# Performance work log

Hardware: AMD Instinct MI355X
Metric: run time of the kernel (lower is better)

Reference implementation:

```python
import jax, jax.numpy as jnp
import numpy as np

B, S, D, H, M = 4, 512, 768, 12, 4
DFF = 4 * D
HD = D // H
EPS = 1e-6  # timm/jvp_layers LayerNorm eps
SCALE = HD ** -0.5


def _ln(x, g, b):
    mu = jnp.mean(x, axis=-1, keepdims=True)
    var = jnp.mean((x - mu) ** 2, axis=-1, keepdims=True)
    return (x - mu) * jax.lax.rsqrt(var + EPS) * g + b


def _block(x, g1, b1, Wqkv, Wproj, bproj, g2, b2, W1, bf1, W2, bf2):
    # pre-norm attention
    h = _ln(x, g1, b1)
    qkv = h @ Wqkv                       # [B,S,3D]
    q, k, v = jnp.split(qkv, 3, axis=-1)
    q = q.reshape(B, S, H, HD)
    k = k.reshape(B, S, H, HD)
    v = v.reshape(B, S, H, HD)
    scores = jnp.einsum('bqhd,bkhd->bhqk', q, k) * SCALE
    attn = jax.nn.softmax(scores, axis=-1)
    o = jnp.einsum('bhqk,bkhd->bqhd', attn, v).reshape(B, S, D)
    x = x + o @ Wproj + bproj
    # pre-norm MLP
    h2 = _ln(x, g2, b2)
    mlp = jax.nn.gelu(h2 @ W1 + bf1, approximate=False) @ W2 + bf2
    return x + mlp


def setup_inputs() -> dict:
    key = jax.random.key(0)
    ks = jax.random.split(key, 8)
    w = 0.02
    return {
        'x': jax.random.normal(ks[0], (B, S, D), jnp.float32),
        'x_tangent': jax.random.normal(ks[1], (B, M, S, D), jnp.float32),
        'g1': jnp.ones((D,), jnp.float32),
        'b1': jnp.zeros((D,), jnp.float32),
        'Wqkv': jax.random.normal(ks[2], (D, 3 * D), jnp.float32) * w,
        'Wproj': jax.random.normal(ks[3], (D, D), jnp.float32) * w,
        'bproj': jnp.zeros((D,), jnp.float32),
        'g2': jnp.ones((D,), jnp.float32),
        'b2': jnp.zeros((D,), jnp.float32),
        'W1': jax.random.normal(ks[4], (D, DFF), jnp.float32) * w,
        'bf1': jnp.zeros((DFF,), jnp.float32),
        'W2': jax.random.normal(ks[5], (DFF, D), jnp.float32) * w,
        'bf2': jnp.zeros((D,), jnp.float32),
    }


def reference(x, x_tangent, g1, b1, Wqkv, Wproj, bproj, g2, b2, W1, bf1, W2, bf2):
    f = lambda xx: _block(xx, g1, b1, Wqkv, Wproj, bproj, g2, b2, W1, bf1, W2, bf2)
    # linearize once: primal + efficient JVP for all M tangent directions
    out, jvp_fn = jax.linearize(f, x)
    out_tangent = jax.vmap(jvp_fn, in_axes=1, out_axes=1)(x_tangent)  # [B,M,S,D]
    return out, out_tangent
```

## Files before the change

### kernel.cpp

```cpp
#include <hip/hip_runtime.h>
#include <math.h>

constexpr int B_ = 4, S_ = 512, D_ = 768, H_ = 12, M_ = 4, DFF_ = 3072, HD_ = 64;
constexpr float EPS_ = 1e-6f;
constexpr float SCALE_ = 0.125f;
constexpr int BS_ = B_ * S_;
constexpr int BH_ = B_ * H_;
constexpr long long BSD_ = (long long)BS_ * D_;
constexpr long long BS3D_ = (long long)BS_ * 3 * D_;
constexpr long long ATT_ = (long long)BH_ * S_ * S_;
constexpr long long BSF_ = (long long)BS_ * DFF_;

typedef __attribute__((ext_vector_type(8))) short bf16x8;
typedef __attribute__((ext_vector_type(4))) float f32x4;

__device__ __forceinline__ ushort f2bf(float f) {
    uint32_t u = __float_as_uint(f);
    u += 0x7FFF + ((u >> 16) & 1);
    return (ushort)(u >> 16);
}
__device__ __forceinline__ float bf2f(ushort u) {
    return __uint_as_float((uint32_t)u << 16);
}

__device__ __forceinline__ void gll16(const ushort* g, ushort* l) {
    __builtin_amdgcn_global_load_lds((const __attribute__((address_space(1))) void*)g,
                                     (__attribute__((address_space(3))) void*)l, 16, 0, 0);
}

template <int N> __device__ __forceinline__ void waitcnt_vm() {
    if constexpr (N == 0) asm volatile("s_waitcnt vmcnt(0)" ::: "memory");
    else if constexpr (N == 4) asm volatile("s_waitcnt vmcnt(4)" ::: "memory");
    else if constexpr (N == 6) asm volatile("s_waitcnt vmcnt(6)" ::: "memory");
    else if constexpr (N == 8) asm volatile("s_waitcnt vmcnt(8)" ::: "memory");
    else static_assert(N == 0 || N == 4 || N == 6 || N == 8, "add literal");
}

__device__ __forceinline__ void waitcnt_lgkm0() {
    asm volatile("s_waitcnt lgkmcnt(0)" ::: "memory");
    __builtin_amdgcn_sched_barrier(0);
}

__device__ __forceinline__ int xcd_swz(int flat, int nwg) {
    int q = nwg >> 3, r = nwg & 7;
    int x = flat & 7, pos = flat >> 3;
    int base = (x < r) ? x * (q + 1) : r * (q + 1) + (x - r) * q;
    return base + pos;
}

__device__ __forceinline__ size_t stroff(int rg, int c, int Nc) {
    int m = rg >> 11;
    int b = (rg >> 9) & (B_ - 1);
    int s = rg & (S_ - 1);
    return ((size_t)((b * M_ + m) * S_ + s)) * Nc + c;
}

__device__ __forceinline__ float block_sum(float v) {
    __shared__ float red[4];
    int tid = threadIdx.x;
#pragma unroll
    for (int off = 32; off > 0; off >>= 1) v += __shfl_down(v, off, 64);
    __syncthreads();
    if ((tid & 63) == 0) red[tid >> 6] = v;
    __syncthreads();
    return red[0] + red[1] + red[2] + red[3];
}

__device__ __forceinline__ float block_max(float v) {
    __shared__ float red[4];
    int tid = threadIdx.x;
#pragma unroll
    for (int off = 32; off > 0; off >>= 1) v = fmaxf(v, __shfl_down(v, off, 64));
    __syncthreads();
    if ((tid & 63) == 0) red[tid >> 6] = v;
    __syncthreads();
    return fmaxf(fmaxf(red[0], red[1]), fmaxf(red[2], red[3]));
}

__global__ __launch_bounds__(256) void transpose_f2b(const float* __restrict__ W,
                                                     ushort* __restrict__ WT,
                                                     int K, int N) {
    __shared__ float t[32][33];
    int n0 = blockIdx.x * 32, k0 = blockIdx.y * 32;
    int tx = threadIdx.x & 31, ty = threadIdx.x >> 5;
#pragma unroll
    for (int i = 0; i < 4; i++)
        t[ty + i * 8][tx] = W[(size_t)(k0 + ty + i * 8) * N + n0 + tx];
    __syncthreads();
#pragma unroll
    for (int i = 0; i < 4; i++)
        WT[(size_t)(n0 + ty + i * 8) * K + k0 + tx] = f2bf(t[tx][ty + i * 8]);
}

__global__ __launch_bounds__(256) void transpose_v(const ushort* __restrict__ src0,
                                                   ushort* __restrict__ dst0) {
    int z = blockIdx.z;
    int m = z / BH_, bh = z % BH_;
    const ushort* qkvb = src0 + (size_t)m * BS3D_;
    ushort* Vt = dst0 + (size_t)m * BSD_;
    int b = bh / H_, hh = bh - b * H_;
    int s0 = blockIdx.x * 32, d0 = blockIdx.y * 32;
    __shared__ ushort t[32][33];
    int tx = threadIdx.x & 31, ty = threadIdx.x >> 5;
#pragma unroll
    for (int i = 0; i < 4; i++)
        t[ty + i * 8][tx] = qkvb[(size_t)(b * S_ + s0 + ty + i * 8) * 3 * D_ + 2 * D_ + hh * HD_ + d0 + tx];
    __syncthreads();
#pragma unroll
    for (int i = 0; i < 4; i++)
        Vt[(size_t)bh * HD_ * S_ + (size_t)(d0 + ty + i * 8) * S_ + s0 + tx] = t[tx][ty + i * 8];
}

__global__ __launch_bounds__(256) void ln_fwd(const float* __restrict__ x,
                                              const float* __restrict__ g,
                                              const float* __restrict__ bta,
                                              ushort* __restrict__ xhat,
                                              ushort* __restrict__ h,
                                              float* __restrict__ rstd) {
    int row = blockIdx.x;
    const float* xr = x + (size_t)row * D_;
    int tid = threadIdx.x;
    float v[3];
    float s = 0.f;
#pragma unroll
    for (int i = 0; i < 3; i++) { v[i] = xr[tid + i * 256]; s += v[i]; }
    s = block_sum(s);
    float mu = s * (1.0f / D_);
    float vs = 0.f;
#pragma unroll
    for (int i = 0; i < 3; i++) { float c = v[i] - mu; vs += c * c; }
    vs = block_sum(vs);
    float rs = rsqrtf(vs * (1.0f / D_) + EPS_);
#pragma unroll
    for (int i = 0; i < 3; i++) {
        int c = tid + i * 256;
        float xh = (v[i] - mu) * rs;
        xhat[(size_t)row * D_ + c] = f2bf(xh);
        h[(size_t)row * D_ + c] = f2bf(xh * g[c] + bta[c]);
    }
    if (tid == 0) rstd[row] = rs;
}

__global__ __launch_bounds__(256) void ln_jvp(const float* __restrict__ tf,
                                              const ushort* __restrict__ tb, int mode,
                                              const ushort* __restrict__ xhat,
                                              const float* __restrict__ rstd,
                                              const float* __restrict__ g,
                                              ushort* __restrict__ dh) {
    int rg = blockIdx.x;
    int r = rg & (BS_ - 1);
    size_t pbase = (size_t)r * D_;
    int tid = threadIdx.x;
    float tv[3], xh[3];
    float s1 = 0.f, s2 = 0.f;
    size_t tbase;
    if (mode == 0) {
        int m = rg >> 11;
        int b = r >> 9, s = r & (S_ - 1);
        tbase = ((size_t)((b * M_ + m) * S_ + s)) * D_;
    } else {
        tbase = (size_t)rg * D_;
    }
#pragma unroll
    for (int i = 0; i < 3; i++) {
        int c = tid + i * 256;
        tv[i] = (mode == 0) ? tf[tbase + c] : bf2f(tb[tbase + c]);
        xh[i] = bf2f(xhat[pbase + c]);
        s1 += tv[i];
        s2 += tv[i] * xh[i];
    }
    s1 = block_sum(s1);
    s2 = block_sum(s2);
    float mt = s1 * (1.0f / D_);
    float mx = s2 * (1.0f / D_);
    float rs = rstd[r];
#pragma unroll
    for (int i = 0; i < 3; i++) {
        int c = tid + i * 256;
        dh[(size_t)rg * D_ + c] = f2bf(g[c] * rs * (tv[i] - mt - xh[i] * mx));
    }
}

template <int BM, int BN, int EPI, bool RS, bool OS>
__global__ __launch_bounds__(256) void gemm_mfma(const ushort* __restrict__ A,
                                                 const ushort* __restrict__ BT,
                                                 const float* __restrict__ bias,
                                                 const float* __restrict__ resf,
                                                 const ushort* __restrict__ resb,
                                                 float* __restrict__ Cf,
                                                 ushort* __restrict__ Cb,
                                                 ushort* __restrict__ aux,
                                                 int Nc, int Kd) {
    constexpr int FI = BM / 32, FJ = BN / 32;
    constexpr int LA = BM / 32, LB = BN / 32, L = LA + LB;
    __shared__ ushort As[2][BM * 64];
    __shared__ ushort Bs[2][BN * 64];
    int tid = threadIdx.x;
    int wave = tid >> 6, lane = tid & 63;
    int wr = wave >> 1, wc = wave & 1;
    int gx = gridDim.x, nwg = gx * gridDim.y;
    int work = xcd_swz(blockIdx.x + blockIdx.y * gx, nwg);
    int band = work / (8 * gx);
    int wi = work - band * (8 * gx);
    int row0 = (band * 8 + (wi & 7)) * BM;
    int col0 = (wi >> 3) * BN;

    int srow = lane >> 3;
    int skel = ((lane & 7) ^ (lane >> 3)) * 8;
    const ushort* Ag0 = A + (size_t)(row0 + srow) * Kd + skel;
    const ushort* Bg0 = BT + (size_t)(col0 + srow) * Kd + skel;

    auto stage = [&](int bufi, int k0) {
#pragma unroll
        for (int cc = 0; cc < LA; cc++) {
            int c = wave * LA + cc;
            gll16(Ag0 + (size_t)(c * 8) * Kd + k0, As[bufi] + c * 512);
        }
#pragma unroll
        for (int cc = 0; cc < LB; cc++) {
            int c = wave * LB + cc;
            gll16(Bg0 + (size_t)(c * 8) * Kd + k0, Bs[bufi] + c * 512);
        }
    };

    int frow = lane & 15, fkb = (lane >> 4) * 8;
    int aoff[2][FI], boff[2][FJ];
#pragma unroll
    for (int ks = 0; ks < 2; ks++) {
        int sw = (fkb + ks * 32) ^ ((frow & 7) * 8);
#pragma unroll
        for (int i = 0; i < FI; i++) aoff[ks][i] = (wr * (BM / 2) + i * 16 + frow) * 64 + sw;
#pragma unroll
        for (int j = 0; j < FJ; j++) boff[ks][j] = (wc * (BN / 2) + j * 16 + frow) * 64 + sw;
    }

    f32x4 acc[FI][FJ] = {};

    int nt = Kd >> 6;
    stage(0, 0);
    if (nt > 1) { stage(1, 64); waitcnt_vm<L>(); }
    else        { waitcnt_vm<0>(); }
    __builtin_amdgcn_s_barrier();
    __builtin_amdgcn_sched_barrier(0);

    int cur = 0;
    for (int t = 0; t < nt; t++) {
        bf16x8 af[2][FI], bfv[2][FJ];
        const ushort* Ab = As[cur];
        const ushort* Bb = Bs[cur];
#pragma unroll
        for (int ks = 0; ks < 2; ks++) {
#pragma unroll
            for (int i = 0; i < FI; i++) af[ks][i] = *(const bf16x8*)(Ab + aoff[ks][i]);
#pragma unroll
            for (int j = 0; j < FJ; j++) bfv[ks][j] = *(const bf16x8*)(Bb + boff[ks][j]);
        }
        waitcnt_lgkm0();
        __builtin_amdgcn_s_barrier();
        if (t + 2 < nt) {
            stage(cur, (t + 2) << 6);
            __builtin_amdgcn_sched_barrier(0);
        }
#pragma unroll
        for (int ks = 0; ks < 2; ks++)
#pragma unroll
            for (int i = 0; i < FI; i++)
#pragma unroll
                for (int j = 0; j < FJ; j++)
                    acc[i][j] = __builtin_amdgcn_mfma_f32_16x16x32_bf16(af[ks][i], bfv[ks][j], acc[i][j], 0, 0, 0);
        __builtin_amdgcn_sched_barrier(0);
        if (t + 2 < nt) waitcnt_vm<L>();
        else if (t + 1 < nt) waitcnt_vm<0>();
        __builtin_amdgcn_s_barrier();
        __builtin_amdgcn_sched_barrier(0);
        cur ^= 1;
    }

#pragma unroll
    for (int i = 0; i < FI; i++) {
        int rbase = row0 + wr * (BM / 2) + i * 16 + (lane >> 4) * 4;
#pragma unroll
        for (int j = 0; j < FJ; j++) {
            int c = col0 + wc * (BN / 2) + j * 16 + (lane & 15);
#pragma unroll
            for (int r = 0; r < 4; r++) {
                int rg = rbase + r;
                size_t off = (size_t)rg * Nc + c;
                float v = acc[i][j][r];
                if (EPI == 0) {
                    if (bias) v += bias[c];
                    if (resf) v += resf[RS ? stroff(rg, c, Nc) : off];
                    if (resb) v += bf2f(resb[off]);
                    if (Cf) { if (OS) Cf[stroff(rg, c, Nc)] = v; else Cf[off] = v; }
                    if (Cb) Cb[off] = f2bf(v);
                } else if (EPI == 1) {
                    v += bias[c];
                    float cdf = 0.5f * (1.0f + erff(v * 0.70710678118654752f));
                    Cb[off] = f2bf(v * cdf);
                    aux[off] = f2bf(cdf + v * 0.39894228040143267f * expf(-0.5f * v * v));
                } else {
                    Cb[off] = f2bf(v * bf2f(aux[(size_t)(rg & (BS_ - 1)) * Nc + c]));
                }
            }
        }
    }
}

template <bool TAN>
__global__ __launch_bounds__(256) void attn_qk_mfma(const ushort* __restrict__ qkvb,
                                                    const ushort* __restrict__ dqkvp,
                                                    ushort* __restrict__ sc) {
    int work = xcd_swz(blockIdx.x, gridDim.x);
    constexpr int NT = S_ / 128;
    int mz = work / (BH_ * NT * NT);
    int rem = work % (BH_ * NT * NT);
    int bh = rem / (NT * NT);
    int r2 = rem % (NT * NT);
    int q0 = (r2 / NT) * 128, kc0 = (r2 % NT) * 128;
    int b = bh / H_, hh = bh - b * H_;
    const size_t qoff = (size_t)b * S_ * 3 * D_ + hh * HD_;
    const int ld = 3 * D_;
    const ushort* dqkv = TAN ? dqkvp + (size_t)mz * BS3D_ : nullptr;
    __shared__ ushort As[128 * 64];
    __shared__ ushort Bs[128 * 64];
    __shared__ ushort dAs[TAN ? 128 * 64 : 1];
    __shared__ ushort dBs[TAN ? 128 * 64 : 1];
    int tid = threadIdx.x;
    int wave = tid >> 6, lane = tid & 63;
    int wr = wave >> 1, wc = wave & 1;

    int srow = lane >> 3;
    int skel = ((lane & 7) ^ (lane >> 3)) * 8;
    const ushort* Ag0 = qkvb + qoff + (size_t)(q0 + srow) * ld + skel;
    const ushort* Bg0 = qkvb + qoff + D_ + (size_t)(kc0 + srow) * ld + skel;

#pragma unroll
    for (int cc = 0; cc < 4; cc++) {
        int c = wave * 4 + cc;
        gll16(Ag0 + (size_t)(c * 8) * ld, As + c * 512);
        gll16(Bg0 + (size_t)(c * 8) * ld, Bs + c * 512);
        if (TAN) {
            gll16(dqkv + qoff + (size_t)(q0 + c * 8 + srow) * ld + skel, dAs + c * 512);
            gll16(dqkv + qoff + D_ + (size_t)(kc0 + c * 8 + srow) * ld + skel, dBs + c * 512);
        }
    }
    __syncthreads();

    int frow = lane & 15, fkb = (lane >> 4) * 8;
    f32x4 acc[4][4] = {};
#pragma unroll
    for (int ks = 0; ks < 2; ks++) {
        int sw = (fkb + ks * 32) ^ ((frow & 7) * 8);
        bf16x8 af[4], bfv[4];
#pragma unroll
        for (int i = 0; i < 4; i++) af[i] = *(const bf16x8*)(As + (wr * 64 + i * 16 + frow) * 64 + sw);
#pragma unroll
        for (int j = 0; j < 4; j++) bfv[j] = *(const bf16x8*)(Bs + (wc * 64 + j * 16 + frow) * 64 + sw);
        if (!TAN) {
#pragma unroll
            for (int i = 0; i < 4; i++)
#pragma unroll
                for (int j = 0; j < 4; j++)
                    acc[i][j] = __builtin_amdgcn_mfma_f32_16x16x32_bf16(af[i], bfv[j], acc[i][j], 0, 0, 0);
        } else {
            bf16x8 daf[4], dbf[4];
#pragma unroll
            for (int i = 0; i < 4; i++) daf[i] = *(const bf16x8*)(dAs + (wr * 64 + i * 16 + frow) * 64 + sw);
#pragma unroll
            for (int j = 0; j < 4; j++) dbf[j] = *(const bf16x8*)(dBs + (wc * 64 + j * 16 + frow) * 64 + sw);
#pragma unroll
            for (int i = 0; i < 4; i++)
#pragma unroll
                for (int j = 0; j < 4; j++) {
                    acc[i][j] = __builtin_amdgcn_mfma_f32_16x16x32_bf16(daf[i], bfv[j], acc[i][j], 0, 0, 0);
                    acc[i][j] = __builtin_amdgcn_mfma_f32_16x16x32_bf16(af[i], dbf[j], acc[i][j], 0, 0, 0);
                }
        }
    }

    ushort* scm = sc + (size_t)mz * ATT_;
#pragma unroll
    for (int i = 0; i < 4; i++) {
        int rbase = q0 + wr * 64 + i * 16 + (lane >> 4) * 4;
#pragma unroll
        for (int j = 0; j < 4; j++) {
            int c = kc0 + wc * 64 + j * 16 + (lane & 15);
#pragma unroll
            for (int r = 0; r < 4; r++)
                scm[((size_t)bh * S_ + rbase + r) * S_ + c] = f2bf(acc[i][j][r] * SCALE_);
        }
    }
}

__global__ __launch_bounds__(256) void attn_av_p(const ushort* __restrict__ Pb,
                                                 const ushort* __restrict__ Vt,
                                                 ushort* __restrict__ outp) {
    int work = xcd_swz(blockIdx.x, gridDim.x);
    constexpr int NT = S_ / 128;
    int bh = work / NT;
    int q0 = (work % NT) * 128;
    int b = bh / H_, hh = bh - b * H_;
    const ushort* Pg = Pb + (size_t)bh * S_ * S_;
    const ushort* Vg = Vt + (size_t)bh * HD_ * S_;
    __shared__ ushort As[128 * 64];
    __shared__ ushort Bs[64 * 64];
    int tid = threadIdx.x;
    int wave = tid >> 6, lane = tid & 63;
    int wr = wave >> 1, wc = wave & 1;
    int srow = lane >> 3;
    int skel = ((lane & 7) ^ (lane >> 3)) * 8;
    int frow = lane & 15, fkb = (lane >> 4) * 8;

    f32x4 acc[4][2] = {};
    for (int k0 = 0; k0 < S_; k0 += 64) {
#pragma unroll
        for (int cc = 0; cc < 4; cc++) {
            int c = wave * 4 + cc;
            gll16(Pg + (size_t)(q0 + c * 8 + srow) * S_ + k0 + skel, As + c * 512);
        }
#pragma unroll
        for (int cc = 0; cc < 2; cc++) {
            int c = wave * 2 + cc;
            gll16(Vg + (size_t)(c * 8 + srow) * S_ + k0 + skel, Bs + c * 512);
        }
        __syncthreads();
#pragma unroll
        for (int ks = 0; ks < 2; ks++) {
            int sw = (fkb + ks * 32) ^ ((frow & 7) * 8);
            bf16x8 af[4], bfv[2];
#pragma unroll
            for (int i = 0; i < 4; i++) af[i] = *(const bf16x8*)(As + (wr * 64 + i * 16 + frow) * 64 + sw);
#pragma unroll
            for (int j = 0; j < 2; j++) bfv[j] = *(const bf16x8*)(Bs + (wc * 32 + j * 16 + frow) * 64 + sw);
#pragma unroll
            for (int i = 0; i < 4; i++)
#pragma unroll
                for (int j = 0; j < 2; j++)
                    acc[i][j] = __builtin_amdgcn_mfma_f32_16x16x32_bf16(af[i], bfv[j], acc[i][j], 0, 0, 0);
        }
        __syncthreads();
    }

#pragma unroll
    for (int i = 0; i < 4; i++) {
        int rbase = q0 + wr * 64 + i * 16 + (lane >> 4) * 4;
#pragma unroll
        for (int j = 0; j < 2; j++) {
            int c = hh * HD_ + wc * 32 + j * 16 + (lane & 15);
#pragma unroll
            for (int r = 0; r < 4; r++)
                outp[(size_t)(b * S_ + rbase + r) * D_ + c] = f2bf(acc[i][j][r]);
        }
    }
}

__global__ __launch_bounds__(256) void attn_av_tan(const ushort* __restrict__ Pb,
                                                   const ushort* __restrict__ dscp,
                                                   const ushort* __restrict__ Vt,
                                                   const ushort* __restrict__ dVtp,
                                                   const ushort* __restrict__ Ob,
                                                   ushort* __restrict__ outp) {
    int work = xcd_swz(blockIdx.x, gridDim.x);
    int mz = work / (BH_ * 4);
    int rem = work % (BH_ * 4);
    int bh = rem / 4;
    int q0 = (rem % 4) * 128;
    int b = bh / H_, hh = bh - b * H_;
    const ushort* Pg = Pb + (size_t)bh * S_ * S_;
    const ushort* Dg = dscp + (size_t)mz * ATT_ + (size_t)bh * S_ * S_;
    const ushort* Vg = Vt + (size_t)bh * HD_ * S_;
    const ushort* dVg = dVtp + (size_t)mz * BSD_ + (size_t)bh * HD_ * S_;
    ushort* outm = outp + (size_t)mz * BSD_;
    __shared__ ushort Ps[128 * 64], Ds[128 * 64], Vs[64 * 64], dVs[64 * 64];
    int tid = threadIdx.x;
    int wave = tid >> 6, lane = tid & 63;
    int wr = wave >> 1, wc = wave & 1;
    int srow = lane >> 3;
    int skel = ((lane & 7) ^ (lane >> 3)) * 8;
    int frow = lane & 15, fkb = (lane >> 4) * 8;
    int aoff[2][4], boff[2][2];
#pragma unroll
    for (int ks = 0; ks < 2; ks++) {
        int sw = (fkb + ks * 32) ^ ((frow & 7) * 8);
#pragma unroll
        for (int i = 0; i < 4; i++) aoff[ks][i] = (wr * 64 + i * 16 + frow) * 64 + sw;
#pragma unroll
        for (int j = 0; j < 2; j++) boff[ks][j] = (wc * 32 + j * 16 + frow) * 64 + sw;
    }

    float s[4] = {0.f, 0.f, 0.f, 0.f};
    f32x4 acc[4][2] = {};

    for (int k0 = 0; k0 < S_; k0 += 64) {
#pragma unroll
        for (int cc = 0; cc < 4; cc++) {
            int c = wave * 4 + cc;
            gll16(Pg + (size_t)(q0 + c * 8 + srow) * S_ + k0 + skel, Ps + c * 512);
            gll16(Dg + (size_t)(q0 + c * 8 + srow) * S_ + k0 + skel, Ds + c * 512);
        }
#pragma unroll
        for (int cc = 0; cc < 2; cc++) {
            int c = wave * 2 + cc;
            gll16(Vg + (size_t)(c * 8 + srow) * S_ + k0 + skel, Vs + c * 512);
            gll16(dVg + (size_t)(c * 8 + srow) * S_ + k0 + skel, dVs + c * 512);
        }
        __syncthreads();
#pragma unroll
        for (int ks = 0; ks < 2; ks++) {
            bf16x8 p8[4], pq8[4], v8[2], dv8[2];
#pragma unroll
            for (int i = 0; i < 4; i++) {
                p8[i] = *(const bf16x8*)(Ps + aoff[ks][i]);
                bf16x8 d8 = *(const bf16x8*)(Ds + aoff[ks][i]);
#pragma unroll
                for (int e = 0; e < 8; e++) {
                    float pd = bf2f((ushort)p8[i][e]) * bf2f((ushort)d8[e]);
                    s[i] += pd;
                    pq8[i][e] = (short)f2bf(pd);
                }
            }
#pragma unroll
            for (int j = 0; j < 2; j++) {
                v8[j] = *(const bf16x8*)(Vs + boff[ks][j]);
                dv8[j] = *(const bf16x8*)(dVs + boff[ks][j]);
            }
#pragma unroll
            for (int i = 0; i < 4; i++)
#pragma unroll
                for (int j = 0; j < 2; j++) {
                    acc[i][j] = __builtin_amdgcn_mfma_f32_16x16x32_bf16(pq8[i], v8[j], acc[i][j], 0, 0, 0);
                    acc[i][j] = __builtin_amdgcn_mfma_f32_16x16x32_bf16(p8[i], dv8[j], acc[i][j], 0, 0, 0);
                }
        }
        __syncthreads();
    }

#pragma unroll
    for (int i = 0; i < 4; i++) {
        s[i] += __shfl_xor(s[i], 16);
        s[i] += __shfl_xor(s[i], 32);
    }

#pragma unroll
    for (int i = 0; i < 4; i++) {
        int rbase = q0 + wr * 64 + i * 16 + (lane >> 4) * 4;
#pragma unroll
        for (int r = 0; r < 4; r++) {
            float sc = __shfl(s[i], ((lane >> 4) << 2) + r);
#pragma unroll
            for (int j = 0; j < 2; j++) {
                int c = hh * HD_ + wc * 32 + j * 16 + (lane & 15);
                float o = bf2f(Ob[(size_t)(b * S_ + rbase + r) * D_ + c]);
                outm[(size_t)(b * S_ + rbase + r) * D_ + c] = f2bf(acc[i][j][r] - sc * o);
            }
        }
    }
}

__global__ __launch_bounds__(256) void softmax_rows(const ushort* __restrict__ sc,
                                                    ushort* __restrict__ scb) {
    size_t row = blockIdx.x;
    const ushort* p = sc + row * S_;
    int tid = threadIdx.x;
    ushort2 vu = *(const ushort2*)&p[tid * 2];
    float v0 = bf2f(vu.x), v1 = bf2f(vu.y);
    float mx = block_max(fmaxf(v0, v1));
    float e0 = expf(v0 - mx), e1 = expf(v1 - mx);
    float s = block_sum(e0 + e1);
    float inv = 1.0f / s;
    ushort2 ob; ob.x = f2bf(e0 * inv); ob.y = f2bf(e1 * inv);
    *(ushort2*)&scb[row * S_ + tid * 2] = ob;
}

extern "C" void kernel_launch(void* const* d_in, const int* in_sizes, int n_in,
                              void* d_out, int out_size, void* d_ws, size_t ws_size,
                              hipStream_t stream) {
    const float* x = (const float*)d_in[0];
    const float* xt = (const float*)d_in[1];
    const float* g1 = (const float*)d_in[2];
    const float* b1 = (const float*)d_in[3];
    const float* Wqkv = (const float*)d_in[4];
    const float* Wproj = (const float*)d_in[5];
    const float* bproj = (const float*)d_in[6];
    const float* g2 = (const float*)d_in[7];
    const float* b2 = (const float*)d_in[8];
    const float* W1 = (const float*)d_in[9];
    const float* bf1 = (const float*)d_in[10];
    const float* W2 = (const float*)d_in[11];
    const float* bf2 = (const float*)d_in[12];
    float* out = (float*)d_out;
    float* out_t = out + BSD_;

    char* wp = (char*)d_ws;
    auto alloc = [&](size_t bytes) { void* p = wp; wp += (bytes + 255) & ~(size_t)255; return p; };
    ushort* xhat1 = (ushort*)alloc(BSD_ * 2);
    ushort* hb = (ushort*)alloc(BSD_ * 2);
    ushort* obb = (ushort*)alloc(BSD_ * 2);
    float* x2 = (float*)alloc(BSD_ * 4);
    ushort* xhat2 = (ushort*)alloc(BSD_ * 2);
    ushort* h2b = (ushort*)alloc(BSD_ * 2);
    ushort* dx2b = (ushort*)alloc(4 * BSD_ * 2);
    ushort* qkvb = (ushort*)alloc(BS3D_ * 2);
    ushort* Vt = (ushort*)alloc(BSD_ * 2);
    ushort* dscb2 = (ushort*)alloc(2 * ATT_ * 2);
    ushort* attnb = (ushort*)alloc(ATT_ * 2);
    ushort* gpb = (ushort*)alloc(BSF_ * 2);
    float* rstd1 = (float*)alloc(BS_ * 4);
    float* rstd2 = (float*)alloc(BS_ * 4);
    ushort* WqkvT = (ushort*)alloc((size_t)D_ * 3 * D_ * 2);
    ushort* WprojT = (ushort*)alloc((size_t)D_ * D_ * 2);
    ushort* W1T = (ushort*)alloc((size_t)DFF_ * D_ * 2);
    ushort* W2T = (ushort*)alloc((size_t)D_ * DFF_ * 2);
    char* regA = (char*)alloc(4 * BSF_ * 2);
    ushort* dqkvb4 = (ushort*)regA;
    ushort* dVt4 = (ushort*)(regA + 4 * BS3D_ * 2);
    ushort* da4 = (ushort*)regA;
    char* regB = (char*)alloc(4 * BSD_ * 2);
    ushort* ab = (ushort*)regB;
    ushort* dh4 = (ushort*)regB;
    ushort* dob4 = (ushort*)regB;
    ushort* dh2_4 = (ushort*)regB;

    transpose_f2b<<<dim3(3 * D_ / 32, D_ / 32), 256, 0, stream>>>(Wqkv, WqkvT, D_, 3 * D_);
    transpose_f2b<<<dim3(D_ / 32, D_ / 32), 256, 0, stream>>>(Wproj, WprojT, D_, D_);
    transpose_f2b<<<dim3(DFF_ / 32, D_ / 32), 256, 0, stream>>>(W1, W1T, D_, DFF_);
    transpose_f2b<<<dim3(D_ / 32, DFF_ / 32), 256, 0, stream>>>(W2, W2T, DFF_, D_);

    ln_fwd<<<BS_, 256, 0, stream>>>(x, g1, b1, xhat1, hb, rstd1);
    gemm_mfma<64, 128, 0, false, false><<<dim3(3 * D_ / 128, BS_ / 64), 256, 0, stream>>>(
        hb, WqkvT, nullptr, nullptr, nullptr, nullptr, qkvb, nullptr, 3 * D_, D_);
    transpose_v<<<dim3(S_ / 32, HD_ / 32, BH_), 256, 0, stream>>>(qkvb, Vt);
    attn_qk_mfma<false><<<(S_ / 128) * (S_ / 128) * BH_, 256, 0, stream>>>(qkvb, nullptr, dscb2);
    softmax_rows<<<BH_ * S_, 256, 0, stream>>>(dscb2, attnb);
    attn_av_p<<<(S_ / 128) * BH_, 256, 0, stream>>>(attnb, Vt, obb);
    gemm_mfma<64, 64, 0, false, false><<<dim3(D_ / 64, BS_ / 64), 256, 0, stream>>>(
        obb, WprojT, bproj, x, nullptr, x2, nullptr, nullptr, D_, D_);
    ln_fwd<<<BS_, 256, 0, stream>>>(x2, g2, b2, xhat2, h2b, rstd2);
    gemm_mfma<128, 128, 1, false, false><<<dim3(DFF_ / 128, BS_ / 128), 256, 0, stream>>>(
        h2b, W1T, bf1, nullptr, nullptr, nullptr, ab, gpb, DFF_, D_);
    gemm_mfma<64, 64, 0, false, false><<<dim3(D_ / 64, BS_ / 64), 256, 0, stream>>>(
        ab, W2T, bf2, x2, nullptr, out, nullptr, nullptr, D_, DFF_);

    ln_jvp<<<4 * BS_, 256, 0, stream>>>(xt, nullptr, 0, xhat1, rstd1, g1, dh4);
    gemm_mfma<128, 128, 0, false, false><<<dim3(3 * D_ / 128, 4 * BS_ / 128), 256, 0, stream>>>(
        dh4, WqkvT, nullptr, nullptr, nullptr, nullptr, dqkvb4, nullptr, 3 * D_, D_);
    transpose_v<<<dim3(S_ / 32, HD_ / 32, 4 * BH_), 256, 0, stream>>>(dqkvb4, dVt4);
    for (int p = 0; p < 2; p++) {
        attn_qk_mfma<true><<<2 * (S_ / 128) * (S_ / 128) * BH_, 256, 0, stream>>>(
            qkvb, dqkvb4 + (size_t)p * 2 * BS3D_, dscb2);
        attn_av_tan<<<2 * 4 * BH_, 256, 0, stream>>>(
            attnb, dscb2, Vt, dVt4 + (size_t)p * 2 * BSD_, obb, dob4 + (size_t)p * 2 * BSD_);
    }
    gemm_mfma<128, 64, 0, true, false><<<dim3(D_ / 64, 4 * BS_ / 128), 256, 0, stream>>>(
        dob4, WprojT, nullptr, xt, nullptr, nullptr, dx2b, nullptr, D_, D_);
    ln_jvp<<<4 * BS_, 256, 0, stream>>>(nullptr, dx2b, 1, xhat2, rstd2, g2, dh2_4);
    gemm_mfma<128, 128, 2, false, false><<<dim3(DFF_ / 128, 4 * BS_ / 128), 256, 0, stream>>>(
        dh2_4, W1T, nullptr, nullptr, nullptr, nullptr, da4, gpb, DFF_, D_);
    gemm_mfma<128, 64, 0, false, true><<<dim3(D_ / 64, 4 * BS_ / 128), 256, 0, stream>>>(
        da4, W2T, nullptr, nullptr, dx2b, out_t, nullptr, nullptr, D_, DFF_);
}
```

Before: 452.1 us.

## Batch primal and tangent QKV projections into one GEMM and V transpose

The first LN-JVP now runs before the primal QKV GEMM, writing its tangents next to the primal LN output so that one GEMM over five row blocks produces both primal and tangent QKV. A single transpose_v launch then produces both Vt and dVt. The LN-JVP also stores a bf16 copy of the input tangent, and the projection GEMM adds that copy as the residual instead of reading the f32 tangent. This removes two launches and the poorly sized 64x128 primal GEMM, but rounds the residual tangent to bf16 and uses more workspace.

```diff
diff --git a/kernel.cpp b/kernel.cpp
--- a/kernel.cpp
+++ b/kernel.cpp
@@ -93,11 +93,12 @@
 }
 
 __global__ __launch_bounds__(256) void transpose_v(const ushort* __restrict__ src0,
-                                                   ushort* __restrict__ dst0) {
+                                                   ushort* __restrict__ Vt0,
+                                                   ushort* __restrict__ dVt4) {
     int z = blockIdx.z;
     int m = z / BH_, bh = z % BH_;
     const ushort* qkvb = src0 + (size_t)m * BS3D_;
-    ushort* Vt = dst0 + (size_t)m * BSD_;
+    ushort* Vt = (m == 0) ? Vt0 : dVt4 + (size_t)(m - 1) * BSD_;
     int b = bh / H_, hh = bh - b * H_;
     int s0 = blockIdx.x * 32, d0 = blockIdx.y * 32;
     __shared__ ushort t[32][33];
@@ -146,7 +147,8 @@
                                               const ushort* __restrict__ xhat,
                                               const float* __restrict__ rstd,
                                               const float* __restrict__ g,
-                                              ushort* __restrict__ dh) {
+                                              ushort* __restrict__ dh,
+                                              ushort* __restrict__ xtb) {
     int rg = blockIdx.x;
     int r = rg & (BS_ - 1);
     size_t pbase = (size_t)r * D_;
@@ -178,6 +180,7 @@
     for (int i = 0; i < 3; i++) {
         int c = tid + i * 256;
         dh[(size_t)rg * D_ + c] = f2bf(g[c] * rs * (tv[i] - mt - xh[i] * mx));
+        if (mode == 0 && xtb) xtb[(size_t)rg * D_ + c] = f2bf(tv[i]);
     }
 }
 
@@ -594,13 +597,13 @@
     char* wp = (char*)d_ws;
     auto alloc = [&](size_t bytes) { void* p = wp; wp += (bytes + 255) & ~(size_t)255; return p; };
     ushort* xhat1 = (ushort*)alloc(BSD_ * 2);
-    ushort* hb = (ushort*)alloc(BSD_ * 2);
+    ushort* hb5 = (ushort*)alloc(5 * BSD_ * 2);
     ushort* obb = (ushort*)alloc(BSD_ * 2);
     float* x2 = (float*)alloc(BSD_ * 4);
     ushort* xhat2 = (ushort*)alloc(BSD_ * 2);
     ushort* h2b = (ushort*)alloc(BSD_ * 2);
     ushort* dx2b = (ushort*)alloc(4 * BSD_ * 2);
-    ushort* qkvb = (ushort*)alloc(BS3D_ * 2);
+    ushort* xt_b = (ushort*)alloc(4 * BSD_ * 2);
     ushort* Vt = (ushort*)alloc(BSD_ * 2);
     ushort* dscb2 = (ushort*)alloc(2 * ATT_ * 2);
     ushort* attnb = (ushort*)alloc(ATT_ * 2);
@@ -612,12 +615,11 @@
     ushort* W1T = (ushort*)alloc((size_t)DFF_ * D_ * 2);
     ushort* W2T = (ushort*)alloc((size_t)D_ * DFF_ * 2);
     char* regA = (char*)alloc(4 * BSF_ * 2);
-    ushort* dqkvb4 = (ushort*)regA;
-    ushort* dVt4 = (ushort*)(regA + 4 * BS3D_ * 2);
+    ushort* qkv5 = (ushort*)regA;
     ushort* da4 = (ushort*)regA;
+    ushort* dVt4 = (ushort*)alloc(4 * BSD_ * 2);
     char* regB = (char*)alloc(4 * BSD_ * 2);
     ushort* ab = (ushort*)regB;
-    ushort* dh4 = (ushort*)regB;
     ushort* dob4 = (ushort*)regB;
     ushort* dh2_4 = (ushort*)regB;
 
@@ -626,11 +628,13 @@
     transpose_f2b<<<dim3(DFF_ / 32, D_ / 32), 256, 0, stream>>>(W1, W1T, D_, DFF_);
     transpose_f2b<<<dim3(D_ / 32, DFF_ / 32), 256, 0, stream>>>(W2, W2T, DFF_, D_);
 
-    ln_fwd<<<BS_, 256, 0, stream>>>(x, g1, b1, xhat1, hb, rstd1);
-    gemm_mfma<64, 128, 0, false, false><<<dim3(3 * D_ / 128, BS_ / 64), 256, 0, stream>>>(
-        hb, WqkvT, nullptr, nullptr, nullptr, nullptr, qkvb, nullptr, 3 * D_, D_);
-    transpose_v<<<dim3(S_ / 32, HD_ / 32, BH_), 256, 0, stream>>>(qkvb, Vt);
-    attn_qk_mfma<false><<<(S_ / 128) * (S_ / 128) * BH_, 256, 0, stream>>>(qkvb, nullptr, dscb2);
+    ln_fwd<<<BS_, 256, 0, stream>>>(x, g1, b1, xhat1, hb5, rstd1);
+    ln_jvp<<<4 * BS_, 256, 0, stream>>>(xt, nullptr, 0, xhat1, rstd1, g1, hb5 + BSD_, xt_b);
+    gemm_mfma<128, 128, 0, false, false><<<dim3(3 * D_ / 128, 5 * BS_ / 128), 256, 0, stream>>>(
+        hb5, WqkvT, nullptr, nullptr, nullptr, nullptr, qkv5, nullptr, 3 * D_, D_);
+    transpose_v<<<dim3(S_ / 32, HD_ / 32, 5 * BH_), 256, 0, stream>>>(qkv5, Vt, dVt4);
+
+    attn_qk_mfma<false><<<(S_ / 128) * (S_ / 128) * BH_, 256, 0, stream>>>(qkv5, nullptr, dscb2);
     softmax_rows<<<BH_ * S_, 256, 0, stream>>>(dscb2, attnb);
     attn_av_p<<<(S_ / 128) * BH_, 256, 0, stream>>>(attnb, Vt, obb);
     gemm_mfma<64, 64, 0, false, false><<<dim3(D_ / 64, BS_ / 64), 256, 0, stream>>>(
@@ -641,19 +645,16 @@
     gemm_mfma<64, 64, 0, false, false><<<dim3(D_ / 64, BS_ / 64), 256, 0, stream>>>(
         ab, W2T, bf2, x2, nullptr, out, nullptr, nullptr, D_, DFF_);
 
-    ln_jvp<<<4 * BS_, 256, 0, stream>>>(xt, nullptr, 0, xhat1, rstd1, g1, dh4);
-    gemm_mfma<128, 128, 0, false, false><<<dim3(3 * D_ / 128, 4 * BS_ / 128), 256, 0, stream>>>(
-        dh4, WqkvT, nullptr, nullptr, nullptr, nullptr, dqkvb4, nullptr, 3 * D_, D_);
-    transpose_v<<<dim3(S_ / 32, HD_ / 32, 4 * BH_), 256, 0, stream>>>(dqkvb4, dVt4);
+    const ushort* dqkv4 = qkv5 + BS3D_;
     for (int p = 0; p < 2; p++) {
         attn_qk_mfma<true><<<2 * (S_ / 128) * (S_ / 128) * BH_, 256, 0, stream>>>(
-            qkvb, dqkvb4 + (size_t)p * 2 * BS3D_, dscb2);
+            qkv5, dqkv4 + (size_t)p * 2 * BS3D_, dscb2);
         attn_av_tan<<<2 * 4 * BH_, 256, 0, stream>>>(
             attnb, dscb2, Vt, dVt4 + (size_t)p * 2 * BSD_, obb, dob4 + (size_t)p * 2 * BSD_);
     }
-    gemm_mfma<128, 64, 0, true, false><<<dim3(D_ / 64, 4 * BS_ / 128), 256, 0, stream>>>(
-        dob4, WprojT, nullptr, xt, nullptr, nullptr, dx2b, nullptr, D_, D_);
-    ln_jvp<<<4 * BS_, 256, 0, stream>>>(nullptr, dx2b, 1, xhat2, rstd2, g2, dh2_4);
+    gemm_mfma<128, 64, 0, false, false><<<dim3(D_ / 64, 4 * BS_ / 128), 256, 0, stream>>>(
+        dob4, WprojT, nullptr, nullptr, xt_b, nullptr, dx2b, nullptr, D_, D_);
+    ln_jvp<<<4 * BS_, 256, 0, stream>>>(nullptr, dx2b, 1, xhat2, rstd2, g2, dh2_4, nullptr);
     gemm_mfma<128, 128, 2, false, false><<<dim3(DFF_ / 128, 4 * BS_ / 128), 256, 0, stream>>>(
         dh2_4, W1T, nullptr, nullptr, nullptr, nullptr, da4, gpb, DFF_, D_);
     gemm_mfma<128, 64, 0, false, true><<<dim3(D_ / 64, 4 * BS_ / 128), 256, 0, stream>>>(
```

After: 443.8 us. About the same (-1.8%).
